# Kernel tuning notes

Measured on AMD Instinct MI355X. Metric: run time of the kernel, lower is better.

## Reference

```python
import jax, jax.numpy as jnp
import numpy as np

HEADS = 8
N_NODES = 16384
DIM = 256
NUM_GLOBAL = 4
E_LOCAL = 131072
E_EXP = 65536


def setup_inputs() -> dict:
    key = jax.random.key(0)
    ks = jax.random.split(key, 8)
    x = jax.random.normal(ks[0], (N_NODES, DIM), dtype=jnp.float32)
    edge_index = jax.random.randint(ks[1], (2, E_LOCAL), 0, N_NODES)
    expander_edge_index = jax.random.randint(ks[2], (2, E_EXP), 0, N_NODES)
    W_qkv = jax.random.normal(ks[3], (DIM, 3 * DIM), dtype=jnp.float32) * (DIM ** -0.5)
    b_qkv = jax.random.normal(ks[4], (3 * DIM,), dtype=jnp.float32) * 0.01
    W_out = jax.random.normal(ks[5], (DIM, DIM), dtype=jnp.float32) * (DIM ** -0.5)
    b_out = jax.random.normal(ks[6], (DIM,), dtype=jnp.float32) * 0.01
    global_tokens = jax.random.normal(ks[7], (NUM_GLOBAL, DIM), dtype=jnp.float32)
    return {"x": x, "edge_index": edge_index,
            "expander_edge_index": expander_edge_index,
            "W_qkv": W_qkv, "b_qkv": b_qkv,
            "W_out": W_out, "b_out": b_out,
            "global_tokens": global_tokens}


def _build_edges(edge_index, expander_edge_index, N, G):
    # local edges + self loops (PyG add_self_loops appends [i,i] edges)
    self_loops = jnp.arange(N)
    nodes = jnp.arange(N)
    gids = jnp.arange(N, N + G)
    # node -> global: meshgrid(arange(N), global_nodes, 'ij') -> src node repeated, dst global tiled
    n2g_src = jnp.repeat(nodes, G)
    n2g_dst = jnp.tile(gids, N)
    src = jnp.concatenate([edge_index[0], self_loops, expander_edge_index[0], n2g_src, n2g_dst])
    dst = jnp.concatenate([edge_index[1], self_loops, expander_edge_index[1], n2g_dst, n2g_src])
    return src, dst


def reference(x, edge_index, expander_edge_index, W_qkv, b_qkv, W_out, b_out, global_tokens):
    N, dim = x.shape
    G = global_tokens.shape[0]
    H = HEADS
    D = dim // H
    total = N + G

    x_full = jnp.concatenate([x, global_tokens], axis=0)          # [N+G, dim]
    qkv = (x_full @ W_qkv + b_qkv).reshape(total, 3, H, D)
    Q, K, V = qkv[:, 0], qkv[:, 1], qkv[:, 2]                     # [N+G, H, D]

    src, dst = _build_edges(edge_index, expander_edge_index, N, G)  # [E]

    scale = D ** -0.5
    scores = (Q[dst] * K[src]).sum(axis=-1) * scale               # [E, H]

    # segment softmax over destination nodes
    m = jax.ops.segment_max(scores, dst, num_segments=total)      # [N+G, H]
    e = jnp.exp(scores - m[dst])                                  # [E, H]
    denom = jax.ops.segment_sum(e, dst, num_segments=total)       # [N+G, H]
    attn = e / denom[dst]                                         # [E, H]

    # scatter-weighted V sum (index_add over dst)
    out = jax.ops.segment_sum(attn[:, :, None] * V[src], dst, num_segments=total)  # [N+G, H, D]
    out = out[:N].reshape(N, H * D)
    return out @ W_out + b_out
```

## Files before the change

### kernel.cpp

```cpp
#include <hip/hip_runtime.h>
#include <hip/hip_bf16.h>
#include <stdint.h>

#define N_NODES   16384
#define DIMM      256
#define HEADS     8
#define HDIM      32
#define NUM_GLOBAL 4
#define N_TOT     (N_NODES + NUM_GLOBAL)
#define E_LOCAL   131072
#define E_EXP     65536
#define E_CSR     (E_LOCAL + E_EXP)
#define ADJ_CAP   64

typedef __hip_bfloat16 bf16;
typedef __attribute__((ext_vector_type(8))) short short8;
typedef __attribute__((ext_vector_type(4))) short sh4;
typedef __attribute__((ext_vector_type(4))) float f32x4;

__device__ __forceinline__ short f2s(float f) {
    bf16 h = __float2bfloat16(f);
    return __builtin_bit_cast(short, h);
}
__device__ __forceinline__ float bu2f(unsigned short u) {
    return __bfloat162float(__builtin_bit_cast(bf16, u));
}

__device__ __forceinline__ int swz(int c, int r) {
    return c ^ (r & 7) ^ ((r >> 3) & 7);
}

__global__ __launch_bounds__(256) void prep_kernel(
    const float* __restrict__ Wqkv, const float* __restrict__ Wout,
    const int* __restrict__ ei, const int* __restrict__ xei,
    const float* __restrict__ x, const float* __restrict__ gtok,
    bf16* __restrict__ Wt1, bf16* __restrict__ Wt2,
    int* __restrict__ cnt, int* __restrict__ adjP, bf16* __restrict__ Xb)
{
    const int b = blockIdx.x;
    const int t = threadIdx.x;
    if (b < 64) {
        __shared__ float T[64][65];
        const float* src; bf16* dst; int n0, k0, ldn;
        if (b < 48) { src = Wqkv; dst = Wt1; n0 = (b % 12) * 64; k0 = (b / 12) * 64; ldn = 768; }
        else        { int bb = b - 48; src = Wout; dst = Wt2; n0 = (bb & 3) * 64; k0 = (bb >> 2) * 64; ldn = 256; }
        #pragma unroll
        for (int i = 0; i < 4; ++i) {
            int idx = t + 256 * i;
            int r = idx >> 4, c4 = (idx & 15) * 4;
            float4 v = *(const float4*)(src + (size_t)(k0 + r) * ldn + n0 + c4);
            T[r][c4] = v.x; T[r][c4 + 1] = v.y; T[r][c4 + 2] = v.z; T[r][c4 + 3] = v.w;
        }
        __syncthreads();
        #pragma unroll
        for (int i = 0; i < 4; ++i) {
            int idx = t + 256 * i;
            int nr = idx >> 4, kk = (idx & 15) * 4;
            sh4 o;
            o[0] = f2s(T[kk][nr]);     o[1] = f2s(T[kk + 1][nr]);
            o[2] = f2s(T[kk + 2][nr]); o[3] = f2s(T[kk + 3][nr]);
            *(sh4*)(dst + (size_t)(n0 + nr) * 256 + k0 + kk) = o;
        }
    } else if (b < 832) {
        int e = (b - 64) * 256 + t;
        int s, d;
        if (e < E_LOCAL)      { s = ei[e];            d = ei[E_LOCAL + e]; }
        else if (e < E_CSR)   { int ee = e - E_LOCAL; s = xei[ee]; d = xei[E_EXP + ee]; }
        else return;
        int pos = atomicAdd(&cnt[d], 1);
        if (pos < ADJ_CAP) adjP[(d << 6) + pos] = s;
    } else {
        int e0 = ((b - 832) * 256 + t) * 8;
        if (e0 < N_TOT * DIMM) {
            int row = e0 >> 8, col = e0 & 255;
            const float* p = (row < N_NODES)
                ? x + (size_t)row * DIMM + col
                : gtok + (size_t)(row - N_NODES) * DIMM + col;
            float4 v0 = *(const float4*)p, v1 = *(const float4*)(p + 4);
            short8 o;
            o[0] = f2s(v0.x); o[1] = f2s(v0.y); o[2] = f2s(v0.z); o[3] = f2s(v0.w);
            o[4] = f2s(v1.x); o[5] = f2s(v1.y); o[6] = f2s(v1.z); o[7] = f2s(v1.w);
            *(short8*)((short*)Xb + (size_t)row * DIMM + col) = o;
        }
    }
}

__global__ __launch_bounds__(256) void qkv_mfma(
    const bf16* __restrict__ Xb, const bf16* __restrict__ Wt,
    const float* __restrict__ bias,
    bf16* __restrict__ Qb, bf16* __restrict__ Kb, bf16* __restrict__ Vb)
{
    const int b = blockIdx.x;
    const int xcd = b & 7;
    const int i = b >> 3;
    const int mt = xcd + 8 * (i / 6);
    if (mt >= 129) return;
    const int m0 = mt * 128;
    const int n0 = (i % 6) * 128;

    __shared__ __align__(16) short SM[32768];
    const int t  = threadIdx.x;
    const int wid = t >> 6, lane = t & 63;
    const int wr = wid >> 1, wc = wid & 1;
    const int lm = lane & 15, lq = lane >> 4;

    f32x4 acc[4][4] = {};
    short8 aregs[4];

    int sr[4], skc[4];
    #pragma unroll
    for (int ii = 0; ii < 4; ++ii) {
        int c8 = t + 256 * ii;
        sr[ii] = c8 >> 3; skc[ii] = c8 & 7;
    }

    #pragma unroll
    for (int ii = 0; ii < 4; ++ii)
        aregs[ii] = *(const short8*)((const short*)Xb + (size_t)(m0 + sr[ii]) * DIMM + skc[ii] * 8);
    #pragma unroll
    for (int ii = 0; ii < 4; ++ii)
        *(short8*)(SM + sr[ii] * 64 + swz(skc[ii], sr[ii]) * 8) = aregs[ii];
    #pragma unroll
    for (int ii = 0; ii < 4; ++ii) {
        short8 v = *(const short8*)((const short*)Wt + (size_t)(n0 + sr[ii]) * 256 + skc[ii] * 8);
        *(short8*)(SM + 8192 + sr[ii] * 64 + swz(skc[ii], sr[ii]) * 8) = v;
    }
    __syncthreads();

    #pragma unroll
    for (int tstep = 0; tstep < 4; ++tstep) {
        const int p = tstep & 1;
        short* As = SM + p * 16384;
        short* Bs = As + 8192;
        if (tstep < 3) {
            const int kn = (tstep + 1) * 64;
            #pragma unroll
            for (int ii = 0; ii < 4; ++ii)
                aregs[ii] = *(const short8*)((const short*)Xb + (size_t)(m0 + sr[ii]) * DIMM + kn + skc[ii] * 8);
        }
        #pragma unroll
        for (int kk = 0; kk < 2; ++kk) {
            const int c = kk * 4 + lq;
            short8 af[4], bfq[4];
            #pragma unroll
            for (int mi = 0; mi < 4; ++mi) {
                int r = wr * 64 + mi * 16 + lm;
                af[mi] = *(const short8*)(As + r * 64 + swz(c, r) * 8);
            }
            #pragma unroll
            for (int ni = 0; ni < 4; ++ni) {
                int n = wc * 64 + ni * 16 + lm;
                bfq[ni] = *(const short8*)(Bs + n * 64 + swz(c, n) * 8);
            }
            #pragma unroll
            for (int mi = 0; mi < 4; ++mi)
                #pragma unroll
                for (int ni = 0; ni < 4; ++ni)
                    acc[mi][ni] = __builtin_amdgcn_mfma_f32_16x16x32_bf16(
                        af[mi], bfq[ni], acc[mi][ni], 0, 0, 0);
        }
        if (tstep < 3) {
            const int kn = (tstep + 1) * 64;
            short* An = SM + (1 - p) * 16384;
            short* Bn = An + 8192;
            __syncthreads();
            #pragma unroll
            for (int ii = 0; ii < 4; ++ii)
                *(short8*)(An + sr[ii] * 64 + swz(skc[ii], sr[ii]) * 8) = aregs[ii];
            #pragma unroll
            for (int ii = 0; ii < 4; ++ii) {
                short8 v = *(const short8*)((const short*)Wt + (size_t)(n0 + sr[ii]) * 256 + kn + skc[ii] * 8);
                *(short8*)(Bn + sr[ii] * 64 + swz(skc[ii], sr[ii]) * 8) = v;
            }
            __syncthreads();
        }
    }

    __syncthreads();
    #pragma unroll
    for (int ni = 0; ni < 4; ++ni) {
        int col = wc * 64 + ni * 16 + lm;
        float bv = bias[n0 + col];
        #pragma unroll
        for (int mi = 0; mi < 4; ++mi) {
            int rowb = wr * 64 + mi * 16 + lq * 4;
            #pragma unroll
            for (int rr = 0; rr < 4; ++rr)
                SM[(rowb + rr) * 136 + col] = f2s(acc[mi][ni][rr] + bv);
        }
    }
    __syncthreads();
    #pragma unroll
    for (int it = 0; it < 8; ++it) {
        int idx = it * 256 + t;
        int r = idx >> 4, c8 = idx & 15;
        int row = m0 + r;
        if (row < N_TOT) {
            int colbase = n0 + (c8 >> 3) * 64;
            int sel = colbase >> 8;
            bf16* __restrict__ dst = (sel == 0) ? Qb : (sel == 1) ? Kb : Vb;
            int cc = (colbase & 255) + (c8 & 7) * 8;
            short8 v = *(const short8*)(SM + r * 136 + c8 * 8);
            *(short8*)((short*)dst + (size_t)row * DIMM + cc) = v;
        }
    }
}

__global__ __launch_bounds__(256) void out_mfma(
    const bf16* __restrict__ O, const bf16* __restrict__ Wt,
    const float* __restrict__ bias, float* __restrict__ out)
{
    const int b = blockIdx.x;
    const int xcd = b & 7;
    const int i = b >> 3;
    const int m0 = (xcd + 8 * (i >> 1)) * 128;
    const int n0 = (i & 1) * 128;

    __shared__ __align__(16) short SM[128 * 136];
    short* As = SM;
    short* Bs = SM + 128 * 64;
    float* CF = (float*)SM;
    const int t  = threadIdx.x;
    const int wid = t >> 6, lane = t & 63;
    const int wr = wid >> 1, wc = wid & 1;
    const int lm = lane & 15, lq = lane >> 4;

    f32x4 acc[4][4] = {};

    for (int k0 = 0; k0 < DIMM; k0 += 64) {
        if (k0) __syncthreads();
        #pragma unroll
        for (int ii = 0; ii < 4; ++ii) {
            int c8 = t + 256 * ii;
            int r  = c8 >> 3, kc = c8 & 7;
            short8 v = *(const short8*)((const short*)O + (size_t)(m0 + r) * DIMM + k0 + kc * 8);
            *(short8*)(As + r * 64 + swz(kc, r) * 8) = v;
        }
        #pragma unroll
        for (int ii = 0; ii < 4; ++ii) {
            int c8 = t + 256 * ii;
            int n  = c8 >> 3, kc = c8 & 7;
            short8 v = *(const short8*)((const short*)Wt + (size_t)(n0 + n) * 256 + k0 + kc * 8);
            *(short8*)(Bs + n * 64 + swz(kc, n) * 8) = v;
        }
        __syncthreads();
        #pragma unroll
        for (int kk = 0; kk < 2; ++kk) {
            const int c = kk * 4 + lq;
            short8 af[4], bfq[4];
            #pragma unroll
            for (int mi = 0; mi < 4; ++mi) {
                int r = wr * 64 + mi * 16 + lm;
                af[mi] = *(const short8*)(As + r * 64 + swz(c, r) * 8);
            }
            #pragma unroll
            for (int ni = 0; ni < 4; ++ni) {
                int n = wc * 64 + ni * 16 + lm;
                bfq[ni] = *(const short8*)(Bs + n * 64 + swz(c, n) * 8);
            }
            #pragma unroll
            for (int mi = 0; mi < 4; ++mi)
                #pragma unroll
                for (int ni = 0; ni < 4; ++ni)
                    acc[mi][ni] = __builtin_amdgcn_mfma_f32_16x16x32_bf16(
                        af[mi], bfq[ni], acc[mi][ni], 0, 0, 0);
        }
    }

    #pragma unroll
    for (int p = 0; p < 2; ++p) {
        __syncthreads();
        if (wr == p) {
            #pragma unroll
            for (int ni = 0; ni < 4; ++ni) {
                int col = wc * 64 + ni * 16 + lm;
                float bv = bias[n0 + col];
                #pragma unroll
                for (int mi = 0; mi < 4; ++mi) {
                    int lr = mi * 16 + lq * 4;
                    #pragma unroll
                    for (int rr = 0; rr < 4; ++rr) {
                        float val = acc[mi][ni][rr] + bv;
                        val = fminf(fmaxf(val, -1e4f), 1e4f);
                        CF[(lr + rr) * 132 + col] = val;
                    }
                }
            }
        }
        __syncthreads();
        #pragma unroll
        for (int it = 0; it < 8; ++it) {
            int idx = it * 256 + t;
            int r = idx >> 5, c4 = idx & 31;
            float4 v = *(const float4*)(CF + r * 132 + c4 * 4);
            *(float4*)(out + (size_t)(m0 + p * 64 + r) * DIMM + n0 + c4 * 4) = v;
        }
    }
}

__global__ __launch_bounds__(256) void attn_kernel(
    const bf16* __restrict__ Qb, const bf16* __restrict__ Kb,
    const bf16* __restrict__ Vb, const int* __restrict__ cnt,
    const int* __restrict__ adjP, bf16* __restrict__ Ob)
{
    const int wave = (blockIdx.x * blockDim.x + threadIdx.x) >> 6;
    const int lane = threadIdx.x & 63;
    if (wave >= N_NODES) return;
    const int n = wave;
    const float scale = 0.1767766952966369f;

    const ushort4* K4 = (const ushort4*)Kb;
    const ushort4* V4 = (const ushort4*)Vb;

    ushort4 qu = ((const ushort4*)Qb)[(size_t)n * 64 + lane];
    float4 q;
    q.x = bu2f(qu.x) * scale; q.y = bu2f(qu.y) * scale;
    q.z = bu2f(qu.z) * scale; q.w = bu2f(qu.w) * scale;

    float4 acc = make_float4(0.f, 0.f, 0.f, 0.f);
    float dsum = 0.f;

    const int deg = min(cnt[n], ADJ_CAP);
    const int* __restrict__ arow = adjP + (n << 6);

    for (int i = -5; i < deg; i += 8) {
        int   sv[8];
        float ok[8];
        #pragma unroll
        for (int u = 0; u < 8; ++u) {
            int ii = i + u;
            bool v = (ii < deg);
            int s = v ? ((ii < 0) ? ((ii == -5) ? n : (N_NODES + ii + 4)) : arow[ii]) : 0;
            sv[u] = min(max(s, 0), N_TOT - 1);
            ok[u] = v ? 1.f : 0.f;
        }
        ushort4 kv[8], vv[8];
        #pragma unroll
        for (int u = 0; u < 8; ++u) kv[u] = K4[(size_t)sv[u] * 64 + lane];
        #pragma unroll
        for (int u = 0; u < 8; ++u) vv[u] = V4[(size_t)sv[u] * 64 + lane];

        float p[8];
        #pragma unroll
        for (int u = 0; u < 8; ++u)
            p[u] = q.x * bu2f(kv[u].x) + q.y * bu2f(kv[u].y)
                 + q.z * bu2f(kv[u].z) + q.w * bu2f(kv[u].w);
        #pragma unroll
        for (int u = 0; u < 8; ++u) {
            p[u] += __shfl_xor(p[u], 1);
            p[u] += __shfl_xor(p[u], 2);
            p[u] += __shfl_xor(p[u], 4);
        }
        #pragma unroll
        for (int u = 0; u < 8; ++u) {
            float wgt = ok[u] * __expf(fminf(p[u], 80.f));
            dsum += wgt;
            acc.x += wgt * bu2f(vv[u].x);
            acc.y += wgt * bu2f(vv[u].y);
            acc.z += wgt * bu2f(vv[u].z);
            acc.w += wgt * bu2f(vv[u].w);
        }
    }

    float r = 1.0f / fmaxf(dsum, 1e-30f);
    ushort4 o;
    o.x = (unsigned short)__builtin_bit_cast(short, __float2bfloat16(fminf(fmaxf(acc.x * r, -500.f), 500.f)));
    o.y = (unsigned short)__builtin_bit_cast(short, __float2bfloat16(fminf(fmaxf(acc.y * r, -500.f), 500.f)));
    o.z = (unsigned short)__builtin_bit_cast(short, __float2bfloat16(fminf(fmaxf(acc.z * r, -500.f), 500.f)));
    o.w = (unsigned short)__builtin_bit_cast(short, __float2bfloat16(fminf(fmaxf(acc.w * r, -500.f), 500.f)));
    ((ushort4*)Ob)[(size_t)n * 64 + lane] = o;
}

extern "C" void kernel_launch(void* const* d_in, const int* in_sizes, int n_in,
                              void* d_out, int out_size, void* d_ws, size_t ws_size,
                              hipStream_t stream)
{
    const float* x    = (const float*)d_in[0];
    const int*   ei   = (const int*)d_in[1];
    const int*   xei  = (const int*)d_in[2];
    const float* Wqkv = (const float*)d_in[3];
    const float* bqkv = (const float*)d_in[4];
    const float* Wout = (const float*)d_in[5];
    const float* bout = (const float*)d_in[6];
    const float* gtok = (const float*)d_in[7];

    int* cnt  = (int*)d_ws;
    int* adjP = cnt + N_NODES;
    uintptr_t fb = ((uintptr_t)(adjP + (size_t)N_NODES * ADJ_CAP) + 15) & ~(uintptr_t)15;
    bf16*  Qb  = (bf16*)fb;
    bf16*  Kb  = Qb + (size_t)N_TOT * DIMM;
    bf16*  Vb  = Kb + (size_t)N_TOT * DIMM;
    bf16*  Ob  = Vb + (size_t)N_TOT * DIMM;
    bf16*  Wt1 = Ob + (size_t)N_NODES * DIMM;
    bf16*  Wt2 = Wt1 + 768 * 256;
    bf16*  Xb  = Wt2 + 256 * 256;

    hipMemsetAsync(cnt, 0, N_NODES * sizeof(int), stream);

    prep_kernel<<<2881, 256, 0, stream>>>(Wqkv, Wout, ei, xei, x, gtok, Wt1, Wt2, cnt, adjP, Xb);
    qkv_mfma<<<816, 256, 0, stream>>>(Xb, Wt1, bqkv, Qb, Kb, Vb);
    attn_kernel<<<N_NODES / 4, 256, 0, stream>>>(Qb, Kb, Vb, cnt, adjP, Ob);
    out_mfma<<<256, 256, 0, stream>>>(Ob, Wt2, bout, (float*)d_out);
}
```

Before: 158.2 us.

## Interleave K/V rows, shrink adjacency to u16, and double-buffer neighbor gathers

The QKV GEMM now writes K and V interleaved per row, so each neighbor's K and V are adjacent in memory. The adjacency list is stored as 16-bit indices and loaded once per wave into lanes, then broadcast with shuffles instead of per-neighbor global loads. The attention loop is software-pipelined with two buffers of 8 neighbor gathers, so loads for the next batch are issued before computing the current one. This aims to hide gather latency and cut index traffic, at the cost of higher register pressure.

```diff
diff --git a/kernel.cpp b/kernel.cpp
--- a/kernel.cpp
+++ b/kernel.cpp
@@ -35,7 +35,7 @@
     const int* __restrict__ ei, const int* __restrict__ xei,
     const float* __restrict__ x, const float* __restrict__ gtok,
     bf16* __restrict__ Wt1, bf16* __restrict__ Wt2,
-    int* __restrict__ cnt, int* __restrict__ adjP, bf16* __restrict__ Xb)
+    int* __restrict__ cnt, unsigned short* __restrict__ adjP, bf16* __restrict__ Xb)
 {
     const int b = blockIdx.x;
     const int t = threadIdx.x;
@@ -68,7 +68,7 @@
         else if (e < E_CSR)   { int ee = e - E_LOCAL; s = xei[ee]; d = xei[E_EXP + ee]; }
         else return;
         int pos = atomicAdd(&cnt[d], 1);
-        if (pos < ADJ_CAP) adjP[(d << 6) + pos] = s;
+        if (pos < ADJ_CAP) adjP[(d << 6) + pos] = (unsigned short)s;
     } else {
         int e0 = ((b - 832) * 256 + t) * 8;
         if (e0 < N_TOT * DIMM) {
@@ -88,7 +88,7 @@
 __global__ __launch_bounds__(256) void qkv_mfma(
     const bf16* __restrict__ Xb, const bf16* __restrict__ Wt,
     const float* __restrict__ bias,
-    bf16* __restrict__ Qb, bf16* __restrict__ Kb, bf16* __restrict__ Vb)
+    bf16* __restrict__ Qb, bf16* __restrict__ KVb)
 {
     const int b = blockIdx.x;
     const int xcd = b & 7;
@@ -198,10 +198,12 @@
         if (row < N_TOT) {
             int colbase = n0 + (c8 >> 3) * 64;
             int sel = colbase >> 8;
-            bf16* __restrict__ dst = (sel == 0) ? Qb : (sel == 1) ? Kb : Vb;
             int cc = (colbase & 255) + (c8 & 7) * 8;
             short8 v = *(const short8*)(SM + r * 136 + c8 * 8);
-            *(short8*)((short*)dst + (size_t)row * DIMM + cc) = v;
+            short* dp;
+            if (sel == 0) dp = (short*)Qb + (size_t)row * DIMM + cc;
+            else          dp = (short*)KVb + (size_t)row * 512 + (sel - 1) * 256 + cc;
+            *(short8*)dp = v;
         }
     }
 }
@@ -299,9 +301,9 @@
 }
 
 __global__ __launch_bounds__(256) void attn_kernel(
-    const bf16* __restrict__ Qb, const bf16* __restrict__ Kb,
-    const bf16* __restrict__ Vb, const int* __restrict__ cnt,
-    const int* __restrict__ adjP, bf16* __restrict__ Ob)
+    const bf16* __restrict__ Qb, const bf16* __restrict__ KVb,
+    const int* __restrict__ cnt, const unsigned short* __restrict__ adjP,
+    bf16* __restrict__ Ob)
 {
     const int wave = (blockIdx.x * blockDim.x + threadIdx.x) >> 6;
     const int lane = threadIdx.x & 63;
@@ -309,42 +311,48 @@
     const int n = wave;
     const float scale = 0.1767766952966369f;
 
-    const ushort4* K4 = (const ushort4*)Kb;
-    const ushort4* V4 = (const ushort4*)Vb;
+    const ushort4* KV4 = (const ushort4*)KVb;
 
     ushort4 qu = ((const ushort4*)Qb)[(size_t)n * 64 + lane];
     float4 q;
     q.x = bu2f(qu.x) * scale; q.y = bu2f(qu.y) * scale;
     q.z = bu2f(qu.z) * scale; q.w = bu2f(qu.w) * scale;
 
+    const int areg = adjP[(n << 6) + lane];
+
+    const int deg = min(cnt[n], ADJ_CAP);
+    const int tot = deg + 5;
+
     float4 acc = make_float4(0.f, 0.f, 0.f, 0.f);
     float dsum = 0.f;
 
-    const int deg = min(cnt[n], ADJ_CAP);
-    const int* __restrict__ arow = adjP + (n << 6);
-
-    for (int i = -5; i < deg; i += 8) {
-        int   sv[8];
-        float ok[8];
+    int svA[8], svB[8];
+    float okA[8], okB[8];
+    ushort4 kA[8], vA[8], kB[8], vB[8];
+
+    auto IDX = [&](int base, int* sv, float* ok) {
         #pragma unroll
         for (int u = 0; u < 8; ++u) {
-            int ii = i + u;
-            bool v = (ii < deg);
-            int s = v ? ((ii < 0) ? ((ii == -5) ? n : (N_NODES + ii + 4)) : arow[ii]) : 0;
-            sv[u] = min(max(s, 0), N_TOT - 1);
-            ok[u] = v ? 1.f : 0.f;
-        }
-        ushort4 kv[8], vv[8];
-        #pragma unroll
-        for (int u = 0; u < 8; ++u) kv[u] = K4[(size_t)sv[u] * 64 + lane];
-        #pragma unroll
-        for (int u = 0; u < 8; ++u) vv[u] = V4[(size_t)sv[u] * 64 + lane];
-
+            int ii = base + u - 5;
+            bool val = (ii < deg);
+            int sg = __shfl(areg, ii & 63);
+            int s  = (ii < 0) ? ((ii == -5) ? n : (N_NODES + ii + 4)) : sg;
+            sv[u] = val ? s : n;
+            ok[u] = val ? 1.f : 0.f;
+        }
+    };
+    auto LOAD = [&](const int* sv, ushort4* kk, ushort4* vv) {
+        #pragma unroll
+        for (int u = 0; u < 8; ++u) kk[u] = KV4[(size_t)sv[u] * 128 + lane];
+        #pragma unroll
+        for (int u = 0; u < 8; ++u) vv[u] = KV4[(size_t)sv[u] * 128 + 64 + lane];
+    };
+    auto PROC = [&](const ushort4* kk, const ushort4* vv, const float* ok) {
         float p[8];
         #pragma unroll
         for (int u = 0; u < 8; ++u)
-            p[u] = q.x * bu2f(kv[u].x) + q.y * bu2f(kv[u].y)
-                 + q.z * bu2f(kv[u].z) + q.w * bu2f(kv[u].w);
+            p[u] = q.x * bu2f(kk[u].x) + q.y * bu2f(kk[u].y)
+                 + q.z * bu2f(kk[u].z) + q.w * bu2f(kk[u].w);
         #pragma unroll
         for (int u = 0; u < 8; ++u) {
             p[u] += __shfl_xor(p[u], 1);
@@ -360,6 +368,18 @@
             acc.z += wgt * bu2f(vv[u].z);
             acc.w += wgt * bu2f(vv[u].w);
         }
+    };
+
+    IDX(0, svA, okA); LOAD(svA, kA, vA);
+    int base = 0;
+    while (true) {
+        if (base + 8 < tot) { IDX(base + 8, svB, okB); LOAD(svB, kB, vB); }
+        PROC(kA, vA, okA);
+        if (base + 8 >= tot) break;
+        if (base + 16 < tot) { IDX(base + 16, svA, okA); LOAD(svA, kA, vA); }
+        PROC(kB, vB, okB);
+        if (base + 16 >= tot) break;
+        base += 16;
     }
 
     float r = 1.0f / fmaxf(dsum, 1e-30f);
@@ -385,12 +405,11 @@
     const float* gtok = (const float*)d_in[7];
 
     int* cnt  = (int*)d_ws;
-    int* adjP = cnt + N_NODES;
+    unsigned short* adjP = (unsigned short*)(cnt + N_NODES);
     uintptr_t fb = ((uintptr_t)(adjP + (size_t)N_NODES * ADJ_CAP) + 15) & ~(uintptr_t)15;
     bf16*  Qb  = (bf16*)fb;
-    bf16*  Kb  = Qb + (size_t)N_TOT * DIMM;
-    bf16*  Vb  = Kb + (size_t)N_TOT * DIMM;
-    bf16*  Ob  = Vb + (size_t)N_TOT * DIMM;
+    bf16*  KVb = Qb + (size_t)N_TOT * DIMM;
+    bf16*  Ob  = KVb + (size_t)N_TOT * 512;
     bf16*  Wt1 = Ob + (size_t)N_NODES * DIMM;
     bf16*  Wt2 = Wt1 + 768 * 256;
     bf16*  Xb  = Wt2 + 256 * 256;
@@ -398,7 +417,7 @@
     hipMemsetAsync(cnt, 0, N_NODES * sizeof(int), stream);
 
     prep_kernel<<<2881, 256, 0, stream>>>(Wqkv, Wout, ei, xei, x, gtok, Wt1, Wt2, cnt, adjP, Xb);
-    qkv_mfma<<<816, 256, 0, stream>>>(Xb, Wt1, bqkv, Qb, Kb, Vb);
-    attn_kernel<<<N_NODES / 4, 256, 0, stream>>>(Qb, Kb, Vb, cnt, adjP, Ob);
+    qkv_mfma<<<816, 256, 0, stream>>>(Xb, Wt1, bqkv, Qb, KVb);
+    attn_kernel<<<N_NODES / 4, 256, 0, stream>>>(Qb, KVb, cnt, adjP, Ob);
     out_mfma<<<256, 256, 0, stream>>>(Ob, Wt2, bout, (float*)d_out);
 }
```

Result: faster. 148.7 us (-6.0%).
